# Optimization experiments

Hardware: AMD Instinct MI355X
Metric: run time of the kernel (lower is better)

## Reference

```python
import jax, jax.numpy as jnp
import numpy as np

B, W, H, C = 8, 32, 32, 64   # batch, width, height, hidden_size (per-head dim)
NH = 8                        # num_attention_heads
P = 64                        # position_encoding_size
M = 32                        # max_position_embeddings
AH = C * NH                   # all_head_size


def setup_inputs() -> dict:
    key = jax.random.key(0)
    ks = jax.random.split(key, 10)
    s = 0.02
    return {
        "hidden_states": jax.random.normal(ks[0], (B, W, H, C), jnp.float32),
        "attention_mask": jnp.zeros((B, W, H), jnp.float32),  # unused by forward (kept for signature parity)
        "row_emb": jax.random.normal(ks[1], (2 * M - 1, P), jnp.float32) * s,
        "col_emb": jax.random.normal(ks[2], (2 * M - 1, P), jnp.float32) * s,
        "w_row": jax.random.normal(ks[3], (NH, P), jnp.float32) * s,  # head_keys_row.weight (no bias)
        "w_col": jax.random.normal(ks[4], (NH, P), jnp.float32) * s,  # head_keys_col.weight (no bias)
        "w_q": jax.random.normal(ks[5], (AH, C), jnp.float32) * s,
        "b_q": jnp.zeros((AH,), jnp.float32),
        "w_k": jax.random.normal(ks[6], (AH, C), jnp.float32) * s,
        "b_k": jnp.zeros((AH,), jnp.float32),
        "w_v": jax.random.normal(ks[7], (C, AH), jnp.float32) * s,  # value: Linear(all_head_size, hidden_size)
        "b_v": jnp.zeros((C,), jnp.float32),
    }


def reference(hidden_states, attention_mask, row_emb, col_emb, w_row, w_col,
              w_q, b_q, w_k, b_k, w_v, b_v):
    b, w, h, c = hidden_states.shape
    nh = w_row.shape[0]
    # relative index table (buffer)
    rel = (jnp.arange(M)[None, :] - jnp.arange(M)[:, None]) + (M - 1)  # (M, M)

    # positional scores
    ri_w = rel[:w, :w].reshape(-1)                                   # (w*w,)
    row_scores = (row_emb[ri_w] @ w_row.T).reshape(1, w, 1, w, nh)   # axis pattern: j,l
    ri_h = rel[:h, :h].reshape(-1)
    col_scores = (col_emb[ri_h] @ w_col.T).reshape(h, 1, h, 1, nh)   # axis pattern: i,k
    pos = (row_scores + col_scores).transpose(0, 1, 4, 2, 3)         # (h, w, nh, h, w)

    # data-dependent scores (use_attention_data=True)
    q = (hidden_states @ w_q.T + b_q).reshape(b, w, h, nh, c)
    k = (hidden_states @ w_k.T + b_k).reshape(b, w, h, nh, c)
    data = jnp.einsum('bijhd,bklhd->bijhkl', q, k) / jnp.sqrt(jnp.float32(c))

    scores = pos[None] + data                                        # (b, w, h, nh, w, h)  (w==h)
    probs = jax.nn.softmax(scores.reshape(b, h, w, nh, h * w), axis=-1)
    probs = probs.reshape(b, h, w, nh, h, w)

    out = jnp.einsum('bijhkl,bkld->bijhd', probs, hidden_states)     # (b, w, h, nh, c)
    out = out.reshape(b, w, h, nh * c)
    return out @ w_v.T + b_v
```

## Files before the change

### kernel.cpp

```cpp
#include <hip/hip_runtime.h>
#include <hip/hip_bf16.h>
#include <cstdint>
#include <cstddef>

#define SB 8
#define SNH 8
#define SS 1024
#define SC 64

typedef __attribute__((ext_vector_type(8)))  short bf16x8;
typedef __attribute__((ext_vector_type(4)))  short bf16x4;
typedef __attribute__((ext_vector_type(4)))  float f32x4;
typedef __attribute__((ext_vector_type(16))) float f32x16;
typedef __attribute__((ext_vector_type(4)))  unsigned u32x4;

#define INVLN2 1.44269504088896f
#define QSCALE (0.125f * INVLN2)

static __device__ __forceinline__ short f2bf(float f) {
    __hip_bfloat16 h = __float2bfloat16(f);
    return __builtin_bit_cast(short, h);
}
static __device__ __forceinline__ float bf2f(short s) {
    return __builtin_bit_cast(float, (unsigned)((unsigned short)s) << 16);
}

static __device__ __forceinline__ bf16x8 cvt8(const float* __restrict__ p, float scl) {
    const float4 a = *(const float4*)p;
    const float4 b = *(const float4*)(p + 4);
    bf16x8 o;
    o[0] = f2bf(a.x * scl); o[1] = f2bf(a.y * scl); o[2] = f2bf(a.z * scl); o[3] = f2bf(a.w * scl);
    o[4] = f2bf(b.x * scl); o[5] = f2bf(b.y * scl); o[6] = f2bf(b.z * scl); o[7] = f2bf(b.w * scl);
    return o;
}
static __device__ __forceinline__ bf16x8 cvt8v(float4 a, float4 b) {
    bf16x8 o;
    o[0] = f2bf(a.x); o[1] = f2bf(a.y); o[2] = f2bf(a.z); o[3] = f2bf(a.w);
    o[4] = f2bf(b.x); o[5] = f2bf(b.y); o[6] = f2bf(b.z); o[7] = f2bf(b.w);
    return o;
}

static __device__ __forceinline__ unsigned pk2(float lo, float hi) {
    return (unsigned)(unsigned short)f2bf(lo) | ((unsigned)(unsigned short)f2bf(hi) << 16);
}

#if __has_builtin(__builtin_amdgcn_permlane32_swap)
typedef __attribute__((ext_vector_type(2))) unsigned uint2v;
static __device__ __forceinline__ void plswap(unsigned& a, unsigned& b) {
    uint2v r = __builtin_amdgcn_permlane32_swap(a, b, false, false);
    a = r[0]; b = r[1];
}
#else
static __device__ __forceinline__ void plswap(unsigned& a, unsigned& b) {
    asm volatile("v_permlane32_swap_b32 %0, %1" : "+v"(a), "+v"(b));
}
#endif

static __device__ __forceinline__ float xhalf_sum(float x) {
    unsigned a = __builtin_bit_cast(unsigned, x), b = a;
    plswap(a, b);
    return __builtin_bit_cast(float, a) + __builtin_bit_cast(float, b);
}

#define MFMA32(a, b, c) __builtin_amdgcn_mfma_f32_32x32x16_bf16((a), (b), (c), 0, 0, 0)

static __device__ __forceinline__ void dlayout_to_bfrag(const float* src, bf16x8* dst) {
#pragma unroll
    for (int k = 0; k < 4; ++k) {
        const int base = (k >> 1) * 16 + (k & 1) * 8;
        unsigned w0 = pk2(src[base + 0], src[base + 1]);
        unsigned w2 = pk2(src[base + 4], src[base + 5]);
        plswap(w0, w2);
        unsigned w1 = pk2(src[base + 2], src[base + 3]);
        unsigned w3 = pk2(src[base + 6], src[base + 7]);
        plswap(w1, w3);
        u32x4 uw; uw[0] = w0; uw[1] = w1; uw[2] = w2; uw[3] = w3;
        dst[k] = __builtin_bit_cast(bf16x8, uw);
    }
}

__global__ __launch_bounds__(256) void prep1(
    const float* __restrict__ row_emb, const float* __restrict__ col_emb,
    const float* __restrict__ w_row,   const float* __restrict__ w_col,
    const float* __restrict__ w_v,  const float* __restrict__ w_q,
    const float* __restrict__ w_k,  const float* __restrict__ hid,
    const float* __restrict__ b_q,  const float* __restrict__ b_k,
    float* __restrict__ posRow, float* __restrict__ posCol,
    short* __restrict__ wvB, short* __restrict__ hidB, short* __restrict__ VtBw,
    short* __restrict__ MqBt, float* __restrict__ row0,
    float* __restrict__ vn, float* __restrict__ snv)
{
    const int bx = blockIdx.x;
    const int tid = threadIdx.x;
    __shared__ float T[64][65];

    if (bx < 64) {
        const int idx = bx * 256 + tid;
        const int which = idx >> 13;
        const int r = idx & 8191;
        const int n = r >> 10;
        const int j = (r >> 5) & 31;
        const int l = r & 31;
        const float* emb = which ? col_emb : row_emb;
        const float* wgt = which ? w_col : w_row;
        const int e = l - j + 31;
        float acc = 0.f;
        for (int p = 0; p < 64; p += 4) {
            const float4 ev = *(const float4*)&emb[e * 64 + p];
            const float4 wv4 = *(const float4*)&wgt[n * 64 + p];
            acc += ev.x * wv4.x + ev.y * wv4.y + ev.z * wv4.z + ev.w * wv4.w;
        }
        (which ? posCol : posRow)[r] = acc * INVLN2;
    } else if (bx < 80) {
        const int t = (bx - 64) * 256 + tid;
        *(bf16x8*)&wvB[t * 8] = cvt8(&w_v[t * 8], 1.0f);
    } else if (bx < 208) {
        const int z = bx - 80;
        const int b = z & 7, kt = z >> 3;
        const int r  = tid >> 2;
        const int c0 = (tid & 3) * 16;
        const float* src = hid + (((size_t)b * 1024) + kt * 64 + r) * 64 + c0;
        const float4 f0 = ((const float4*)src)[0];
        const float4 f1 = ((const float4*)src)[1];
        const float4 f2 = ((const float4*)src)[2];
        const float4 f3 = ((const float4*)src)[3];
        T[r][c0 + 0] = f0.x; T[r][c0 + 1] = f0.y; T[r][c0 + 2] = f0.z; T[r][c0 + 3] = f0.w;
        T[r][c0 + 4] = f1.x; T[r][c0 + 5] = f1.y; T[r][c0 + 6] = f1.z; T[r][c0 + 7] = f1.w;
        T[r][c0 + 8] = f2.x; T[r][c0 + 9] = f2.y; T[r][c0 +10] = f2.z; T[r][c0 +11] = f2.w;
        T[r][c0 +12] = f3.x; T[r][c0 +13] = f3.y; T[r][c0 +14] = f3.z; T[r][c0 +15] = f3.w;
        short* hb = hidB + (((size_t)b * 1024) + kt * 64 + r) * 64 + c0;
        *(bf16x8*)(hb)     = cvt8v(f0, f1);
        *(bf16x8*)(hb + 8) = cvt8v(f2, f3);
        __syncthreads();
        short* tbase = VtBw + ((size_t)(b * 16 + kt)) * 4096;
#pragma unroll
        for (int it = 0; it < 2; ++it) {
            const int d  = (tid >> 3) + 32 * it;
            const int k0 = (tid & 7) * 8;
            bf16x8 o;
#pragma unroll
            for (int j = 0; j < 8; ++j) o[j] = f2bf(T[k0 + j][d]);
            *(bf16x8*)&tbase[d * 64 + k0] = o;
        }
    } else {
        const int n = bx - 208;
        const int wv = tid >> 6;
        const int lane = tid & 63;
        if (wv == 0) {
            const int h = lane >> 5, qc = lane & 31;
            bf16x8 afr[2][4], bfr[2][4];
#pragma unroll
            for (int ct = 0; ct < 2; ++ct)
#pragma unroll
                for (int k = 0; k < 4; ++k) {
                    bf16x8 oa, ob;
#pragma unroll
                    for (int j = 0; j < 8; ++j) {
                        const int a = 16 * k + 8 * h + j;
                        oa[j] = f2bf(w_q[(size_t)(n * 64 + a) * 64 + 32 * ct + qc] * QSCALE);
                        ob[j] = f2bf(w_k[(size_t)(n * 64 + a) * 64 + 32 * ct + qc]);
                    }
                    afr[ct][k] = oa; bfr[ct][k] = ob;
                }
#pragma unroll
            for (int ct1 = 0; ct1 < 2; ++ct1)
#pragma unroll
                for (int ctc = 0; ctc < 2; ++ctc) {
                    f32x16 d;
#pragma unroll
                    for (int i = 0; i < 16; ++i) d[i] = 0.f;
                    d = MFMA32(afr[ct1][0], bfr[ctc][0], d);
                    d = MFMA32(afr[ct1][1], bfr[ctc][1], d);
                    d = MFMA32(afr[ct1][2], bfr[ctc][2], d);
                    d = MFMA32(afr[ct1][3], bfr[ctc][3], d);
                    short* mb = MqBt + n * 4096 + (32 * ctc + qc) * 64 + 32 * ct1 + 4 * h;
#pragma unroll
                    for (int rg = 0; rg < 4; ++rg) {
                        bf16x4 ov;
                        ov[0] = f2bf(d[4 * rg + 0]); ov[1] = f2bf(d[4 * rg + 1]);
                        ov[2] = f2bf(d[4 * rg + 2]); ov[3] = f2bf(d[4 * rg + 3]);
                        *(bf16x4*)&mb[8 * rg] = ov;
                    }
                }
        } else if (wv == 1) {
            const int c2 = lane;
            float acc = 0.f;
            for (int a = 0; a < 64; ++a)
                acc += b_q[n * 64 + a] * w_k[(size_t)(n * 64 + a) * 64 + c2];
            row0[n * 64 + c2] = acc * QSCALE;
        } else if (wv == 2) {
            const int c1 = lane;
            float acc = 0.f;
            for (int a = 0; a < 64; ++a)
                acc += b_k[n * 64 + a] * w_q[(size_t)(n * 64 + a) * 64 + c1];
            vn[n * 64 + c1] = acc * QSCALE;
        } else {
            float p = b_q[n * 64 + lane] * b_k[n * 64 + lane];
#pragma unroll
            for (int o = 1; o < 64; o <<= 1) p += __shfl_xor(p, o);
            if (lane == 0) snv[n] = p * QSCALE;
        }
    }
}

__global__ __launch_bounds__(256, 2) void attn_mfma(
    const short* __restrict__ hidB, const short* __restrict__ VtBw,
    const short* __restrict__ MqBt, const float* __restrict__ row0,
    const float* __restrict__ vn,   const float* __restrict__ snv,
    const float* __restrict__ posRow, const float* __restrict__ posCol,
    short* __restrict__ hoB)
{
    const int orig = blockIdx.x;
    const int swzb = (orig & 7) * 64 + (orig >> 3);
    const int b    = swzb >> 6;
    const int n    = (swzb >> 3) & 7;
    const int qblk = swzb & 7;

    const int tid  = threadIdx.x;
    const int w    = tid >> 6;
    const int lane = tid & 63;
    const int h    = lane >> 5;
    const int qc   = lane & 31;
    const int qt   = qblk * 4 + w;
    const int q    = qt * 32 + qc;
    const int swz  = qc & 7;

    __shared__ __align__(16) short KtA[4096], KtB[4096];
    __shared__ __align__(16) short VtA[4096], VtB_s[4096];

    bf16x8 qf[4];
    float cq;
    {
        const short* hrow = hidB + (((size_t)b * 1024) + q) * 64 + 8 * h;
        bf16x8 hq[4];
#pragma unroll
        for (int kk = 0; kk < 4; ++kk) hq[kk] = *(const bf16x8*)(hrow + 16 * kk);

        float aD[32];
#pragma unroll
        for (int ct = 0; ct < 2; ++ct) {
            f32x16 ci;
            const float* r0p = row0 + n * 64 + 32 * ct + 4 * h;
#pragma unroll
            for (int rg = 0; rg < 4; ++rg) {
                const float4 v = *(const float4*)(r0p + 8 * rg);
                ci[4 * rg + 0] = v.x; ci[4 * rg + 1] = v.y;
                ci[4 * rg + 2] = v.z; ci[4 * rg + 3] = v.w;
            }
            const short* mbase = MqBt + n * 4096 + (size_t)(32 * ct + qc) * 64 + 8 * h;
            ci = MFMA32(*(const bf16x8*)(mbase),      hq[0], ci);
            ci = MFMA32(*(const bf16x8*)(mbase + 16), hq[1], ci);
            ci = MFMA32(*(const bf16x8*)(mbase + 32), hq[2], ci);
            ci = MFMA32(*(const bf16x8*)(mbase + 48), hq[3], ci);
#pragma unroll
            for (int i = 0; i < 16; ++i) aD[16 * ct + i] = ci[i];
        }
        dlayout_to_bfrag(aD, qf);

        float part = 0.f;
#pragma unroll
        for (int kk = 0; kk < 4; ++kk) {
            const float4 v0 = *(const float4*)&vn[n * 64 + 16 * kk + 8 * h];
            const float4 v1 = *(const float4*)&vn[n * 64 + 16 * kk + 8 * h + 4];
            part += bf2f(hq[kk][0]) * v0.x + bf2f(hq[kk][1]) * v0.y +
                    bf2f(hq[kk][2]) * v0.z + bf2f(hq[kk][3]) * v0.w +
                    bf2f(hq[kk][4]) * v1.x + bf2f(hq[kk][5]) * v1.y +
                    bf2f(hq[kk][6]) * v1.z + bf2f(hq[kk][7]) * v1.w;
        }
        cq = xhalf_sum(part) + snv[n];
    }

    float prowA[16];
    {
        const float* pr = posRow + (n * 32 + qc) * 32 + 4 * h;
#pragma unroll
        for (int rg = 0; rg < 4; ++rg) {
            const float4 v = *(const float4*)(pr + 8 * rg);
            prowA[4 * rg + 0] = v.x + cq; prowA[4 * rg + 1] = v.y + cq;
            prowA[4 * rg + 2] = v.z + cq; prowA[4 * rg + 3] = v.w + cq;
        }
    }
    const float* pcp = posCol + (n * 32 + qt) * 32;

    const short* Kbase = hidB + (size_t)b * 65536;
    const short* Vbase = VtBw + ((size_t)b * 16) * 4096;

    const int c16 = tid & 7;
    const int srow = tid >> 3;
    const int woffA = srow * 128 + ((c16 ^ (srow & 7)) << 4);
    const int woffB = (srow + 32) * 128 + ((c16 ^ (srow & 7)) << 4);
    const short* kp0 = Kbase + (size_t)srow * 64 + c16 * 8;
    const short* kp1 = Kbase + (size_t)(srow + 32) * 64 + c16 * 8;
    const short* vp0 = Vbase + (size_t)srow * 64 + c16 * 8;
    const short* vp1 = Vbase + (size_t)(srow + 32) * 64 + c16 * 8;

    float lsum = 0.f;
    f32x16 oacc[2];
#pragma unroll
    for (int dt = 0; dt < 2; ++dt)
#pragma unroll
        for (int i = 0; i < 16; ++i) oacc[dt][i] = 0.f;

    auto compute = [&](int kt, const short* Ktc_s, const short* Vtc_s) {
        const char* Ktc = (const char*)Ktc_s;
        const char* Vtc = (const char*)Vtc_s;
        const float pc0 = pcp[2 * kt];
        const float pc1 = pcp[2 * kt + 1];

        bf16x8 kf[2][4];
#pragma unroll
        for (int ct = 0; ct < 2; ++ct) {
            const int rb = (32 * ct + qc) * 128;
#pragma unroll
            for (int k = 0; k < 4; ++k)
                kf[ct][k] = *(const bf16x8*)(Ktc + rb + (((2 * k + h) ^ swz) << 4));
        }

        f32x16 sc[2];
#pragma unroll
        for (int ct = 0; ct < 2; ++ct) {
            const float pc = ct ? pc1 : pc0;
            f32x16 ci;
#pragma unroll
            for (int i = 0; i < 16; ++i) ci[i] = prowA[i] + pc;
            ci = MFMA32(kf[ct][0], qf[0], ci);
            ci = MFMA32(kf[ct][1], qf[1], ci);
            ci = MFMA32(kf[ct][2], qf[2], ci);
            sc[ct] = MFMA32(kf[ct][3], qf[3], ci);
        }

        bf16x8 vf[2][4];
#pragma unroll
        for (int dt = 0; dt < 2; ++dt) {
            const int rb = (32 * dt + qc) * 128;
#pragma unroll
            for (int ks = 0; ks < 4; ++ks)
                vf[dt][ks] = *(const bf16x8*)(Vtc + rb + (((2 * ks + h) ^ swz) << 4));
        }

        float p[32];
#pragma unroll
        for (int i = 0; i < 16; ++i) {
            p[i]      = __builtin_amdgcn_exp2f(sc[0][i]);
            p[16 + i] = __builtin_amdgcn_exp2f(sc[1][i]);
        }
        float s8[8];
#pragma unroll
        for (int i = 0; i < 8; ++i)
            s8[i] = (p[i] + p[i + 8]) + (p[16 + i] + p[24 + i]);
        lsum += ((s8[0] + s8[1]) + (s8[2] + s8[3])) +
                ((s8[4] + s8[5]) + (s8[6] + s8[7]));

        bf16x8 pfrag[4];
        dlayout_to_bfrag(p, pfrag);

#pragma unroll
        for (int dt = 0; dt < 2; ++dt) {
            f32x16 oa = oacc[dt];
            oa = MFMA32(vf[dt][0], pfrag[0], oa);
            oa = MFMA32(vf[dt][1], pfrag[1], oa);
            oa = MFMA32(vf[dt][2], pfrag[2], oa);
            oacc[dt] = MFMA32(vf[dt][3], pfrag[3], oa);
        }
    };

    {
        const float4 ka  = *(const float4*)kp0;
        const float4 kb4 = *(const float4*)kp1;
        const float4 va  = *(const float4*)vp0;
        const float4 vb4 = *(const float4*)vp1;
        *(float4*)((char*)KtA + woffA) = ka;
        *(float4*)((char*)KtA + woffB) = kb4;
        *(float4*)((char*)VtA + woffA) = va;
        *(float4*)((char*)VtA + woffB) = vb4;
    }
    __syncthreads();

#pragma unroll 1
    for (int pr = 0; pr < 8; ++pr) {
        const int kt0 = 2 * pr, kt1 = kt0 + 1;
        {
            const size_t o = (size_t)(kt0 + 1) * 4096;
            const float4 ka  = *(const float4*)(kp0 + o);
            const float4 kb4 = *(const float4*)(kp1 + o);
            const float4 va  = *(const float4*)(vp0 + o);
            const float4 vb4 = *(const float4*)(vp1 + o);
            compute(kt0, KtA, VtA);
            *(float4*)((char*)KtB + woffA) = ka;
            *(float4*)((char*)KtB + woffB) = kb4;
            *(float4*)((char*)VtB_s + woffA) = va;
            *(float4*)((char*)VtB_s + woffB) = vb4;
            __syncthreads();
        }
        if (kt1 < 15) {
            const size_t o = (size_t)(kt1 + 1) * 4096;
            const float4 ka  = *(const float4*)(kp0 + o);
            const float4 kb4 = *(const float4*)(kp1 + o);
            const float4 va  = *(const float4*)(vp0 + o);
            const float4 vb4 = *(const float4*)(vp1 + o);
            compute(kt1, KtB, VtB_s);
            *(float4*)((char*)KtA + woffA) = ka;
            *(float4*)((char*)KtA + woffB) = kb4;
            *(float4*)((char*)VtA + woffA) = va;
            *(float4*)((char*)VtA + woffB) = vb4;
            __syncthreads();
        } else {
            compute(kt1, KtB, VtB_s);
        }
    }

    const float inv = 1.0f / xhalf_sum(lsum);
    short* orow = hoB + ((size_t)(b * 1024 + q)) * 512 + n * 64 + 4 * h;
#pragma unroll
    for (int dt = 0; dt < 2; ++dt)
#pragma unroll
        for (int rg = 0; rg < 4; ++rg) {
            bf16x4 ov;
            ov[0] = f2bf(oacc[dt][4 * rg + 0] * inv);
            ov[1] = f2bf(oacc[dt][4 * rg + 1] * inv);
            ov[2] = f2bf(oacc[dt][4 * rg + 2] * inv);
            ov[3] = f2bf(oacc[dt][4 * rg + 3] * inv);
            *(bf16x4*)&orow[32 * dt + 8 * rg] = ov;
        }
}

__global__ __launch_bounds__(64) void v_proj(
    const short* __restrict__ hoB, const short* __restrict__ wvB,
    const float* __restrict__ bv, float* __restrict__ out)
{
    const int bo = blockIdx.x;
    const int bx = (bo & 7) * 64 + (bo >> 3);
    const int lane = threadIdx.x;
    const int g  = lane >> 4;
    const int qi = lane & 15;
    const int row0 = bx * 16;

    const short* arow = hoB + (size_t)(row0 + qi) * 512 + 8 * g;

    f32x4 acc[4];
#pragma unroll
    for (int ct = 0; ct < 4; ++ct) acc[ct] = (f32x4){0.f, 0.f, 0.f, 0.f};

#pragma unroll 4
    for (int ks = 0; ks < 16; ++ks) {
        const bf16x8 af = *(const bf16x8*)(arow + ks * 32);
#pragma unroll
        for (int ct = 0; ct < 4; ++ct) {
            const bf16x8 bfr = *(const bf16x8*)(wvB + (size_t)(16 * ct + qi) * 512 + ks * 32 + 8 * g);
            acc[ct] = __builtin_amdgcn_mfma_f32_16x16x32_bf16(af, bfr, acc[ct], 0, 0, 0);
        }
    }

#pragma unroll
    for (int ct = 0; ct < 4; ++ct) {
        const float bias = bv[16 * ct + qi];
#pragma unroll
        for (int r = 0; r < 4; ++r)
            out[(size_t)(row0 + 4 * g + r) * 64 + 16 * ct + qi] = acc[ct][r] + bias;
    }
}

extern "C" void kernel_launch(void* const* d_in, const int* in_sizes, int n_in,
                              void* d_out, int out_size, void* d_ws, size_t ws_size,
                              hipStream_t stream)
{
    const float* hid     = (const float*)d_in[0];
    const float* row_emb = (const float*)d_in[2];
    const float* col_emb = (const float*)d_in[3];
    const float* w_row   = (const float*)d_in[4];
    const float* w_col   = (const float*)d_in[5];
    const float* w_q     = (const float*)d_in[6];
    const float* b_q     = (const float*)d_in[7];
    const float* w_k     = (const float*)d_in[8];
    const float* b_k     = (const float*)d_in[9];
    const float* w_v     = (const float*)d_in[10];
    const float* b_v     = (const float*)d_in[11];
    float* out = (float*)d_out;

    short* hidB   = (short*)d_ws;
    short* VtBw   = hidB + (size_t)SB * SS * SC;
    short* MqBt   = VtBw + (size_t)SB * SS * SC;
    float* posRow = (float*)(MqBt + SNH * SC * SC);
    float* posCol = posRow + SNH * 32 * 32;
    float* row0   = posCol + SNH * 32 * 32;
    float* vn     = row0 + SNH * SC;
    float* snv    = vn + SNH * SC;
    short* wvB    = (short*)(snv + 8);
    short* hoB    = wvB + (size_t)SC * SNH * SC;

    prep1<<<216, 256, 0, stream>>>(row_emb, col_emb, w_row, w_col, w_v, w_q,
                                   w_k, hid, b_q, b_k,
                                   posRow, posCol, wvB, hidB, VtBw,
                                   MqBt, row0, vn, snv);
    attn_mfma<<<512, 256, 0, stream>>>(hidB, VtBw, MqBt, row0, vn, snv,
                                       posRow, posCol, hoB);
    v_proj<<<512, 64, 0, stream>>>(hoB, wvB, b_v, out);
}
```

Baseline: 48.18 us.

## Stage K/V tiles two at a time and raise wave priority around MFMAs

```diff
diff --git a/kernel.cpp b/kernel.cpp
--- a/kernel.cpp
+++ b/kernel.cpp
@@ -225,8 +225,8 @@
     const int q    = qt * 32 + qc;
     const int swz  = qc & 7;
 
-    __shared__ __align__(16) short KtA[4096], KtB[4096];
-    __shared__ __align__(16) short VtA[4096], VtB_s[4096];
+    __shared__ __align__(16) short Kb0[4096], Kb1[4096], Kb2[4096], Kb3[4096];
+    __shared__ __align__(16) short Vb0[4096], Vb1[4096], Vb2[4096], Vb3[4096];
 
     bf16x8 qf[4];
     float cq;
@@ -316,6 +316,7 @@
                 kf[ct][k] = *(const bf16x8*)(Ktc + rb + (((2 * k + h) ^ swz) << 4));
         }
 
+        __builtin_amdgcn_s_setprio(1);
         f32x16 sc[2];
 #pragma unroll
         for (int ct = 0; ct < 2; ++ct) {
@@ -328,6 +329,7 @@
             ci = MFMA32(kf[ct][2], qf[2], ci);
             sc[ct] = MFMA32(kf[ct][3], qf[3], ci);
         }
+        __builtin_amdgcn_s_setprio(0);
 
         bf16x8 vf[2][4];
 #pragma unroll
@@ -354,6 +356,7 @@
         bf16x8 pfrag[4];
         dlayout_to_bfrag(p, pfrag);
 
+        __builtin_amdgcn_s_setprio(1);
 #pragma unroll
         for (int dt = 0; dt < 2; ++dt) {
             f32x16 oa = oacc[dt];
@@ -362,50 +365,79 @@
             oa = MFMA32(vf[dt][2], pfrag[2], oa);
             oacc[dt] = MFMA32(vf[dt][3], pfrag[3], oa);
         }
+        __builtin_amdgcn_s_setprio(0);
     };
 
     {
-        const float4 ka  = *(const float4*)kp0;
-        const float4 kb4 = *(const float4*)kp1;
-        const float4 va  = *(const float4*)vp0;
-        const float4 vb4 = *(const float4*)vp1;
-        *(float4*)((char*)KtA + woffA) = ka;
-        *(float4*)((char*)KtA + woffB) = kb4;
-        *(float4*)((char*)VtA + woffA) = va;
-        *(float4*)((char*)VtA + woffB) = vb4;
+        const float4 a0 = *(const float4*)kp0;
+        const float4 a1 = *(const float4*)kp1;
+        const float4 a2 = *(const float4*)vp0;
+        const float4 a3 = *(const float4*)vp1;
+        const float4 b0 = *(const float4*)(kp0 + 4096);
+        const float4 b1 = *(const float4*)(kp1 + 4096);
+        const float4 b2 = *(const float4*)(vp0 + 4096);
+        const float4 b3 = *(const float4*)(vp1 + 4096);
+        *(float4*)((char*)Kb0 + woffA) = a0;
+        *(float4*)((char*)Kb0 + woffB) = a1;
+        *(float4*)((char*)Vb0 + woffA) = a2;
+        *(float4*)((char*)Vb0 + woffB) = a3;
+        *(float4*)((char*)Kb1 + woffA) = b0;
+        *(float4*)((char*)Kb1 + woffB) = b1;
+        *(float4*)((char*)Vb1 + woffA) = b2;
+        *(float4*)((char*)Vb1 + woffB) = b3;
     }
     __syncthreads();
 
 #pragma unroll 1
-    for (int pr = 0; pr < 8; ++pr) {
-        const int kt0 = 2 * pr, kt1 = kt0 + 1;
+    for (int j = 0; j < 4; ++j) {
         {
-            const size_t o = (size_t)(kt0 + 1) * 4096;
-            const float4 ka  = *(const float4*)(kp0 + o);
-            const float4 kb4 = *(const float4*)(kp1 + o);
-            const float4 va  = *(const float4*)(vp0 + o);
-            const float4 vb4 = *(const float4*)(vp1 + o);
-            compute(kt0, KtA, VtA);
-            *(float4*)((char*)KtB + woffA) = ka;
-            *(float4*)((char*)KtB + woffB) = kb4;
-            *(float4*)((char*)VtB_s + woffA) = va;
-            *(float4*)((char*)VtB_s + woffB) = vb4;
+            const size_t oA = (size_t)(4 * j + 2) * 4096;
+            const size_t oB = (size_t)(4 * j + 3) * 4096;
+            const float4 a0 = *(const float4*)(kp0 + oA);
+            const float4 a1 = *(const float4*)(kp1 + oA);
+            const float4 a2 = *(const float4*)(vp0 + oA);
+            const float4 a3 = *(const float4*)(vp1 + oA);
+            const float4 b0 = *(const float4*)(kp0 + oB);
+            const float4 b1 = *(const float4*)(kp1 + oB);
+            const float4 b2 = *(const float4*)(vp0 + oB);
+            const float4 b3 = *(const float4*)(vp1 + oB);
+            compute(4 * j,     Kb0, Vb0);
+            compute(4 * j + 1, Kb1, Vb1);
+            *(float4*)((char*)Kb2 + woffA) = a0;
+            *(float4*)((char*)Kb2 + woffB) = a1;
+            *(float4*)((char*)Vb2 + woffA) = a2;
+            *(float4*)((char*)Vb2 + woffB) = a3;
+            *(float4*)((char*)Kb3 + woffA) = b0;
+            *(float4*)((char*)Kb3 + woffB) = b1;
+            *(float4*)((char*)Vb3 + woffA) = b2;
+            *(float4*)((char*)Vb3 + woffB) = b3;
             __syncthreads();
         }
-        if (kt1 < 15) {
-            const size_t o = (size_t)(kt1 + 1) * 4096;
-            const float4 ka  = *(const float4*)(kp0 + o);
-            const float4 kb4 = *(const float4*)(kp1 + o);
-            const float4 va  = *(const float4*)(vp0 + o);
-            const float4 vb4 = *(const float4*)(vp1 + o);
-            compute(kt1, KtB, VtB_s);
-            *(float4*)((char*)KtA + woffA) = ka;
-            *(float4*)((char*)KtA + woffB) = kb4;
-            *(float4*)((char*)VtA + woffA) = va;
-            *(float4*)((char*)VtA + woffB) = vb4;
+        if (j < 3) {
+            const size_t oA = (size_t)(4 * j + 4) * 4096;
+            const size_t oB = (size_t)(4 * j + 5) * 4096;
+            const float4 a0 = *(const float4*)(kp0 + oA);
+            const float4 a1 = *(const float4*)(kp1 + oA);
+            const float4 a2 = *(const float4*)(vp0 + oA);
+            const float4 a3 = *(const float4*)(vp1 + oA);
+            const float4 b0 = *(const float4*)(kp0 + oB);
+            const float4 b1 = *(const float4*)(kp1 + oB);
+            const float4 b2 = *(const float4*)(vp0 + oB);
+            const float4 b3 = *(const float4*)(vp1 + oB);
+            compute(4 * j + 2, Kb2, Vb2);
+            compute(4 * j + 3, Kb3, Vb3);
+            *(float4*)((char*)Kb0 + woffA) = a0;
+            *(float4*)((char*)Kb0 + woffB) = a1;
+            *(float4*)((char*)Vb0 + woffA) = a2;
+            *(float4*)((char*)Vb0 + woffB) = a3;
+            *(float4*)((char*)Kb1 + woffA) = b0;
+            *(float4*)((char*)Kb1 + woffB) = b1;
+            *(float4*)((char*)Vb1 + woffA) = b2;
+            *(float4*)((char*)Vb1 + woffB) = b3;
             __syncthreads();
         } else {
-            compute(kt1, KtB, VtB_s);
+            compute(14, Kb2, Vb2);
+            compute(15, Kb3, Vb3);
         }
     }
 
```

Measured after the change: 58.29 us. 1.21x slower.

## Split attention key range across two wave groups per block with LDS reduction

Applied to the files above, without the earlier changes.

```diff
diff --git a/kernel.cpp b/kernel.cpp
--- a/kernel.cpp
+++ b/kernel.cpp
@@ -68,6 +68,21 @@
 #pragma unroll
     for (int k = 0; k < 4; ++k) {
         const int base = (k >> 1) * 16 + (k & 1) * 8;
+        unsigned w0 = pk2(src[base + 0], src[base + 1]);
+        unsigned w2 = pk2(src[base + 4], src[base + 5]);
+        plswap(w0, w2);
+        unsigned w1 = pk2(src[base + 2], src[base + 3]);
+        unsigned w3 = pk2(src[base + 6], src[base + 7]);
+        plswap(w1, w3);
+        u32x4 uw; uw[0] = w0; uw[1] = w1; uw[2] = w2; uw[3] = w3;
+        dst[k] = __builtin_bit_cast(bf16x8, uw);
+    }
+}
+
+static __device__ __forceinline__ void dhalf_to_bfrag(const float* src, bf16x8* dst) {
+#pragma unroll
+    for (int k = 0; k < 2; ++k) {
+        const int base = k * 8;
         unsigned w0 = pk2(src[base + 0], src[base + 1]);
         unsigned w2 = pk2(src[base + 4], src[base + 5]);
         plswap(w0, w2);
@@ -203,7 +218,7 @@
     }
 }
 
-__global__ __launch_bounds__(256, 2) void attn_mfma(
+__global__ __launch_bounds__(512, 2) void attn_mfma(
     const short* __restrict__ hidB, const short* __restrict__ VtBw,
     const short* __restrict__ MqBt, const float* __restrict__ row0,
     const float* __restrict__ vn,   const float* __restrict__ snv,
@@ -219,14 +234,18 @@
     const int tid  = threadIdx.x;
     const int w    = tid >> 6;
     const int lane = tid & 63;
+    const int grp  = tid >> 8;
     const int h    = lane >> 5;
     const int qc   = lane & 31;
-    const int qt   = qblk * 4 + w;
+    const int qt   = qblk * 4 + (w & 3);
     const int q    = qt * 32 + qc;
     const int swz  = qc & 7;
 
-    __shared__ __align__(16) short KtA[4096], KtB[4096];
-    __shared__ __align__(16) short VtA[4096], VtB_s[4096];
+    __shared__ __align__(16) short lds[32768];
+    short* const Kst0 = lds + (size_t)grp * 16384;
+    short* const Vst0 = Kst0 + 4096;
+    short* const Kst1 = Kst0 + 8192;
+    short* const Vst1 = Kst0 + 12288;
 
     bf16x8 qf[4];
     float cq;
@@ -282,11 +301,12 @@
     }
     const float* pcp = posCol + (n * 32 + qt) * 32;
 
-    const short* Kbase = hidB + (size_t)b * 65536;
-    const short* Vbase = VtBw + ((size_t)b * 16) * 4096;
-
-    const int c16 = tid & 7;
-    const int srow = tid >> 3;
+    const short* Kbase = hidB + (size_t)b * 65536 + (size_t)grp * 8 * 4096;
+    const short* Vbase = VtBw + (size_t)b * 65536 + (size_t)grp * 8 * 4096;
+
+    const int st   = tid & 255;
+    const int c16  = st & 7;
+    const int srow = st >> 3;
     const int woffA = srow * 128 + ((c16 ^ (srow & 7)) << 4);
     const int woffB = (srow + 32) * 128 + ((c16 ^ (srow & 7)) << 4);
     const short* kp0 = Kbase + (size_t)srow * 64 + c16 * 8;
@@ -304,29 +324,34 @@
     auto compute = [&](int kt, const short* Ktc_s, const short* Vtc_s) {
         const char* Ktc = (const char*)Ktc_s;
         const char* Vtc = (const char*)Vtc_s;
-        const float pc0 = pcp[2 * kt];
-        const float pc1 = pcp[2 * kt + 1];
-
-        bf16x8 kf[2][4];
+        const float pcv[2] = {pcp[2 * kt], pcp[2 * kt + 1]};
+
+        bf16x8 pfrag[4];
 #pragma unroll
         for (int ct = 0; ct < 2; ++ct) {
+            bf16x8 kf[4];
             const int rb = (32 * ct + qc) * 128;
 #pragma unroll
             for (int k = 0; k < 4; ++k)
-                kf[ct][k] = *(const bf16x8*)(Ktc + rb + (((2 * k + h) ^ swz) << 4));
-        }
-
-        f32x16 sc[2];
-#pragma unroll
-        for (int ct = 0; ct < 2; ++ct) {
-            const float pc = ct ? pc1 : pc0;
+                kf[k] = *(const bf16x8*)(Ktc + rb + (((2 * k + h) ^ swz) << 4));
+
             f32x16 ci;
 #pragma unroll
-            for (int i = 0; i < 16; ++i) ci[i] = prowA[i] + pc;
-            ci = MFMA32(kf[ct][0], qf[0], ci);
-            ci = MFMA32(kf[ct][1], qf[1], ci);
-            ci = MFMA32(kf[ct][2], qf[2], ci);
-            sc[ct] = MFMA32(kf[ct][3], qf[3], ci);
+            for (int i = 0; i < 16; ++i) ci[i] = prowA[i] + pcv[ct];
+            ci = MFMA32(kf[0], qf[0], ci);
+            ci = MFMA32(kf[1], qf[1], ci);
+            ci = MFMA32(kf[2], qf[2], ci);
+            ci = MFMA32(kf[3], qf[3], ci);
+
+            float p[16];
+#pragma unroll
+            for (int i = 0; i < 16; ++i) p[i] = __builtin_amdgcn_exp2f(ci[i]);
+            float s8[8];
+#pragma unroll
+            for (int i = 0; i < 8; ++i) s8[i] = p[i] + p[i + 8];
+            lsum += ((s8[0] + s8[1]) + (s8[2] + s8[3])) +
+                    ((s8[4] + s8[5]) + (s8[6] + s8[7]));
+            dhalf_to_bfrag(p, &pfrag[2 * ct]);
         }
 
         bf16x8 vf[2][4];
@@ -337,23 +362,6 @@
             for (int ks = 0; ks < 4; ++ks)
                 vf[dt][ks] = *(const bf16x8*)(Vtc + rb + (((2 * ks + h) ^ swz) << 4));
         }
-
-        float p[32];
-#pragma unroll
-        for (int i = 0; i < 16; ++i) {
-            p[i]      = __builtin_amdgcn_exp2f(sc[0][i]);
-            p[16 + i] = __builtin_amdgcn_exp2f(sc[1][i]);
-        }
-        float s8[8];
-#pragma unroll
-        for (int i = 0; i < 8; ++i)
-            s8[i] = (p[i] + p[i + 8]) + (p[16 + i] + p[24 + i]);
-        lsum += ((s8[0] + s8[1]) + (s8[2] + s8[3])) +
-                ((s8[4] + s8[5]) + (s8[6] + s8[7]));
-
-        bf16x8 pfrag[4];
-        dlayout_to_bfrag(p, pfrag);
-
 #pragma unroll
         for (int dt = 0; dt < 2; ++dt) {
             f32x16 oa = oacc[dt];
@@ -364,64 +372,81 @@
         }
     };
 
+    const int kt0a = grp * 8;
+
     {
-        const float4 ka  = *(const float4*)kp0;
-        const float4 kb4 = *(const float4*)kp1;
-        const float4 va  = *(const float4*)vp0;
-        const float4 vb4 = *(const float4*)vp1;
-        *(float4*)((char*)KtA + woffA) = ka;
-        *(float4*)((char*)KtA + woffB) = kb4;
-        *(float4*)((char*)VtA + woffA) = va;
-        *(float4*)((char*)VtA + woffB) = vb4;
+        const float4 a0 = *(const float4*)kp0;
+        const float4 a1 = *(const float4*)kp1;
+        const float4 a2 = *(const float4*)vp0;
+        const float4 a3 = *(const float4*)vp1;
+        *(float4*)((char*)Kst0 + woffA) = a0;
+        *(float4*)((char*)Kst0 + woffB) = a1;
+        *(float4*)((char*)Vst0 + woffA) = a2;
+        *(float4*)((char*)Vst0 + woffB) = a3;
     }
     __syncthreads();
 
 #pragma unroll 1
-    for (int pr = 0; pr < 8; ++pr) {
-        const int kt0 = 2 * pr, kt1 = kt0 + 1;
+    for (int pr = 0; pr < 4; ++pr) {
+        const int j0 = 2 * pr, j1 = j0 + 1;
         {
-            const size_t o = (size_t)(kt0 + 1) * 4096;
-            const float4 ka  = *(const float4*)(kp0 + o);
-            const float4 kb4 = *(const float4*)(kp1 + o);
-            const float4 va  = *(const float4*)(vp0 + o);
-            const float4 vb4 = *(const float4*)(vp1 + o);
-            compute(kt0, KtA, VtA);
-            *(float4*)((char*)KtB + woffA) = ka;
-            *(float4*)((char*)KtB + woffB) = kb4;
-            *(float4*)((char*)VtB_s + woffA) = va;
-            *(float4*)((char*)VtB_s + woffB) = vb4;
+            const size_t o = (size_t)(j0 + 1) * 4096;
+            const float4 a0 = *(const float4*)(kp0 + o);
+            const float4 a1 = *(const float4*)(kp1 + o);
+            const float4 a2 = *(const float4*)(vp0 + o);
+            const float4 a3 = *(const float4*)(vp1 + o);
+            compute(kt0a + j0, Kst0, Vst0);
+            *(float4*)((char*)Kst1 + woffA) = a0;
+            *(float4*)((char*)Kst1 + woffB) = a1;
+            *(float4*)((char*)Vst1 + woffA) = a2;
+            *(float4*)((char*)Vst1 + woffB) = a3;
             __syncthreads();
         }
-        if (kt1 < 15) {
-            const size_t o = (size_t)(kt1 + 1) * 4096;
-            const float4 ka  = *(const float4*)(kp0 + o);
-            const float4 kb4 = *(const float4*)(kp1 + o);
-            const float4 va  = *(const float4*)(vp0 + o);
-            const float4 vb4 = *(const float4*)(vp1 + o);
-            compute(kt1, KtB, VtB_s);
-            *(float4*)((char*)KtA + woffA) = ka;
-            *(float4*)((char*)KtA + woffB) = kb4;
-            *(float4*)((char*)VtA + woffA) = va;
-            *(float4*)((char*)VtA + woffB) = vb4;
+        if (j1 < 7) {
+            const size_t o = (size_t)(j1 + 1) * 4096;
+            const float4 a0 = *(const float4*)(kp0 + o);
+            const float4 a1 = *(const float4*)(kp1 + o);
+            const float4 a2 = *(const float4*)(vp0 + o);
+            const float4 a3 = *(const float4*)(vp1 + o);
+            compute(kt0a + j1, Kst1, Vst1);
+            *(float4*)((char*)Kst0 + woffA) = a0;
+            *(float4*)((char*)Kst0 + woffB) = a1;
+            *(float4*)((char*)Vst0 + woffA) = a2;
+            *(float4*)((char*)Vst0 + woffB) = a3;
             __syncthreads();
         } else {
-            compute(kt1, KtB, VtB_s);
-        }
-    }
-
-    const float inv = 1.0f / xhalf_sum(lsum);
-    short* orow = hoB + ((size_t)(b * 1024 + q)) * 512 + n * 64 + 4 * h;
-#pragma unroll
-    for (int dt = 0; dt < 2; ++dt)
-#pragma unroll
-        for (int rg = 0; rg < 4; ++rg) {
-            bf16x4 ov;
-            ov[0] = f2bf(oacc[dt][4 * rg + 0] * inv);
-            ov[1] = f2bf(oacc[dt][4 * rg + 1] * inv);
-            ov[2] = f2bf(oacc[dt][4 * rg + 2] * inv);
-            ov[3] = f2bf(oacc[dt][4 * rg + 3] * inv);
-            *(bf16x4*)&orow[32 * dt + 8 * rg] = ov;
-        }
+            compute(kt0a + j1, Kst1, Vst1);
+        }
+    }
+
+    __syncthreads();
+    float* cb = (float*)lds;
+    const int slot = ((w & 3) * 64 + lane) * 34;
+    if (grp == 1) {
+#pragma unroll
+        for (int i = 0; i < 16; ++i) { cb[slot + i] = oacc[0][i]; cb[slot + 16 + i] = oacc[1][i]; }
+        cb[slot + 32] = lsum;
+    }
+    __syncthreads();
+    if (grp == 0) {
+#pragma unroll
+        for (int i = 0; i < 16; ++i) { oacc[0][i] += cb[slot + i]; oacc[1][i] += cb[slot + 16 + i]; }
+        lsum += cb[slot + 32];
+
+        const float inv = 1.0f / xhalf_sum(lsum);
+        short* orow = hoB + ((size_t)(b * 1024 + q)) * 512 + n * 64 + 4 * h;
+#pragma unroll
+        for (int dt = 0; dt < 2; ++dt)
+#pragma unroll
+            for (int rg = 0; rg < 4; ++rg) {
+                bf16x4 ov;
+                ov[0] = f2bf(oacc[dt][4 * rg + 0] * inv);
+                ov[1] = f2bf(oacc[dt][4 * rg + 1] * inv);
+                ov[2] = f2bf(oacc[dt][4 * rg + 2] * inv);
+                ov[3] = f2bf(oacc[dt][4 * rg + 3] * inv);
+                *(bf16x4*)&orow[32 * dt + 8 * rg] = ov;
+            }
+    }
 }
 
 __global__ __launch_bounds__(64) void v_proj(
@@ -492,7 +517,7 @@
                                    w_k, hid, b_q, b_k,
                                    posRow, posCol, wvB, hidB, VtBw,
                                    MqBt, row0, vn, snv);
-    attn_mfma<<<512, 256, 0, stream>>>(hidB, VtBw, MqBt, row0, vn, snv,
+    attn_mfma<<<512, 512, 0, stream>>>(hidB, VtBw, MqBt, row0, vn, snv,
                                        posRow, posCol, hoB);
     v_proj<<<512, 64, 0, stream>>>(hoB, wvB, b_v, out);
 }
```

After: 54.00 us. +12.1%, slower.
